# Performance work log

Measured on AMD Instinct MI355X. Metric: run time of the kernel, lower is better.

## Reference

```python
import jax, jax.numpy as jnp
import numpy as np

HEAD_COUNT = 16
HEAD_DIM = 128  # embed_count // head_count = 2048 // 16


def setup_inputs() -> dict:
    key = jax.random.key(0)
    k0, k1, k2, k3, k4 = jax.random.split(key, 5)
    B, C, S = 4, 2048, 1024
    keys = jax.random.normal(k0, (B, C, 1, S), dtype=jnp.float32)
    values = jax.random.normal(k1, (B, C, 1, S), dtype=jnp.float32)
    queries = jax.random.normal(k2, (B, C, 1, S), dtype=jnp.float32)
    attention_mask = jax.random.randint(k3, (B, S), 0, 2).astype(bool)
    # guarantee at least one valid key per batch row so softmax is finite
    attention_mask = attention_mask.at[:, 0].set(True)
    w_out = jax.random.normal(k4, (C, C), dtype=jnp.float32) * 0.02
    return {"keys": keys, "values": values, "queries": queries,
            "attention_mask": attention_mask, "w_out": w_out}


def reference(keys, values, queries, attention_mask, w_out):
    B, C, _, S = keys.shape
    h, d = HEAD_COUNT, HEAD_DIM
    # keys: [B,C,1,S] -> transpose(1,3) -> [B,S,1,C] -> [B,S,h,d]
    k = jnp.transpose(keys[:, :, 0, :], (0, 2, 1)).reshape(B, S, h, d)      # bkhd
    # values/queries: [B,C,1,S] -> [B,h,d,S] -> transpose(1,2) -> [B,d,h,S]
    v = jnp.transpose(values[:, :, 0, :].reshape(B, h, d, S), (0, 2, 1, 3))  # bdhk
    q = jnp.transpose(queries[:, :, 0, :].reshape(B, h, d, S), (0, 2, 1, 3)) # bdhq
    # additive mask bias: 0 where attended, -inf where masked; broadcast over h,q
    bias = jnp.where(attention_mask, 0.0, -jnp.inf).astype(keys.dtype)       # [B,K]
    scale = 1.0 / np.sqrt(d).astype(np.float32)
    w = jnp.einsum('bdhq,bkhd->bkhq', q * scale, k)                          # [B,K,h,Q]
    w = w + bias[:, :, None, None]
    w = jax.nn.softmax(w, axis=1)  # softmax over keys (dim 1)
    hid = jnp.einsum('bkhq,bdhk->bdhq', w, v)                                # [B,d,h,Q]
    hid = jnp.transpose(hid, (0, 2, 1, 3)).reshape(B, C, S)                  # [B,C,Q]
    out = jnp.einsum('oc,bcq->boq', w_out, hid)                              # 1x1 conv out_proj
    return out.reshape(B, C, 1, S)
```

## Files before the change

### kernel.cpp

```cpp
#include <hip/hip_runtime.h>

#define Bq 4
#define Cc 2048
#define Ss 1024
#define Hh 16
#define Dd 128

#define QSCALE 0.127517429f

typedef __bf16 bf16x8 __attribute__((ext_vector_type(8)));
typedef float  f32x4  __attribute__((ext_vector_type(4)));

__device__ __forceinline__ ushort f2bf(float f) {
    uint u = __float_as_uint(f);
    u += 0x7FFFu + ((u >> 16) & 1u);
    return (ushort)(u >> 16);
}
__device__ __forceinline__ uint pack2bf(float a, float b) {
    return (uint)f2bf(a) | ((uint)f2bf(b) << 16);
}
__device__ __forceinline__ void gld16(const void* g, void* l) {
    __builtin_amdgcn_global_load_lds(
        (const __attribute__((address_space(1))) unsigned int*)g,
        (__attribute__((address_space(3))) unsigned int*)l, 16, 0, 0);
}

__global__ __launch_bounds__(256) void mask_bias_k(const unsigned* __restrict__ mask,
                                                   float* __restrict__ bias) {
    __shared__ int f01, ff;
    const int t = threadIdx.x;
    if (t == 0) { f01 = 0; ff = 0; }
    __syncthreads();
    int a = 0, b = 0;
    for (int i = t; i < 1024; i += 256) {
        unsigned v = mask[i];
        if (v != 0u && v != 1u) a = 1;
        if (v != 0u && v != 0x3F800000u) b = 1;
    }
    if (a) atomicOr(&f01, 1);
    if (b) atomicOr(&ff, 1);
    __syncthreads();
    const int mode = f01 ? (ff ? 1 : 2) : 0;
    const int* mi = (const int*)mask;
    const unsigned char* mb = (const unsigned char*)mask;
    const float* mf = (const float*)mask;
    for (int i = t; i < Bq * Ss; i += 256) {
        bool on;
        if (mode == 0)      on = (mi[i] != 0);
        else if (mode == 1) on = (mb[i] != 0);
        else                on = (mf[i] != 0.0f);
        bias[i] = on ? 0.0f : -1e30f;
    }
}

__global__ __launch_bounds__(256) void wcvt_swz(const float* __restrict__ w,
                                                ushort* __restrict__ wb) {
    const size_t e = ((size_t)blockIdx.x * 256 + threadIdx.x) * 8;
    const int row = (int)(e >> 11), col = (int)(e & 2047);
    const int colS = (col & ~63) | ((col & 63) ^ ((row & 7) << 3));
    float4 v0 = *(const float4*)&w[e];
    float4 v1 = *(const float4*)&w[e + 4];
    uint4 o;
    o.x = pack2bf(v0.x, v0.y); o.y = pack2bf(v0.z, v0.w);
    o.z = pack2bf(v1.x, v1.y); o.w = pack2bf(v1.z, v1.w);
    *(uint4*)&wb[(size_t)row * 2048 + colS] = o;
}

__global__ __launch_bounds__(256) void vcvt_perm(const float* __restrict__ v,
                                                 ushort* __restrict__ vb) {
    const int tid = blockIdx.x * 256 + threadIdx.x;
    const int row = tid >> 7;
    const int cp = tid & 127;
    const int blk = (cp >> 3) * 64, x = cp & 7, kk0 = 2 * x;
    const float* src = v + (size_t)row * 1024 + blk;
    float a0 = src[kk0], a1 = src[16 + kk0], a2 = src[32 + kk0], a3 = src[48 + kk0];
    float b0 = src[kk0 + 1], b1 = src[17 + kk0], b2 = src[33 + kk0], b3 = src[49 + kk0];
    uint4 o;
    o.x = pack2bf(a0, a1); o.y = pack2bf(a2, a3);
    o.z = pack2bf(b0, b1); o.w = pack2bf(b2, b3);
    *(uint4*)&vb[(size_t)row * 1024 + blk + ((kk0 * 4) ^ ((row & 7) << 3))] = o;
}

__global__ __launch_bounds__(256) void qk_prep(const float* __restrict__ queries,
                                               const float* __restrict__ keys,
                                               ushort* __restrict__ Qt,
                                               ushort* __restrict__ Kt) {
    __shared__ float T[128][65];
    const int t = threadIdx.x;
    const int s0 = blockIdx.x * 64;
    const int bh = blockIdx.y;
    const int isK = blockIdx.z;
    const float* src = (isK ? keys : queries) + (size_t)bh * 128 * 1024;
    const float sc = isK ? 1.0f : QSCALE;

#pragma unroll
    for (int p = 0; p < 8; ++p) {
        const int d = p * 16 + (t >> 4);
        float4 v = *(const float4*)&src[(size_t)d * 1024 + s0 + (t & 15) * 4];
        T[d][(t & 15) * 4 + 0] = v.x * sc;
        T[d][(t & 15) * 4 + 1] = v.y * sc;
        T[d][(t & 15) * 4 + 2] = v.z * sc;
        T[d][(t & 15) * 4 + 3] = v.w * sc;
    }
    __syncthreads();

    ushort* outp = isK ? Kt : Qt;
#pragma unroll
    for (int p = 0; p < 4; ++p) {
        const int k = p * 16 + (t >> 4);
        const int x = t & 15;
        uint4 o;
        o.x = pack2bf(T[x * 8 + 0][k], T[x * 8 + 1][k]);
        o.y = pack2bf(T[x * 8 + 2][k], T[x * 8 + 3][k]);
        o.z = pack2bf(T[x * 8 + 4][k], T[x * 8 + 5][k]);
        o.w = pack2bf(T[x * 8 + 6][k], T[x * 8 + 7][k]);
        const size_t rowbyte = ((size_t)bh * 1024 + s0 + k) * 256;
        const int boff = isK ? ((x * 16) ^ ((k & 7) << 4)) : (x * 16);
        *(uint4*)((char*)outp + rowbyte + boff) = o;
    }
}

__global__ __launch_bounds__(512) void attn3(const ushort* __restrict__ Qt,
                                             const ushort* __restrict__ Kt,
                                             const ushort* __restrict__ Vbf,
                                             const float* __restrict__ bias,
                                             ushort* __restrict__ hidT) {
    __shared__ __align__(16) char SMEM[103424];
    ushort* KT2  = (ushort*)SMEM;
    ushort* Vs2  = (ushort*)(SMEM + 32768);
    ushort* PTb  = (ushort*)(SMEM + 65536);
    float*  biasS = (float*)(SMEM + 98304);
    float*  lbuf  = (float*)(SMEM + 102400);

    const int t = threadIdx.x, l = t & 63, w = t >> 6;
    const int kk = l & 15, g = l >> 4;

    const int bid = blockIdx.x;
    const int vid = (bid & 7) * 32 + (bid >> 3);
    const int bh = vid >> 2, qt = vid & 3;
    const int b = bh >> 4;
    const int q0 = qt * 256;
    const size_t bhbase = (size_t)bh * 1024;

    for (int i = t; i < Ss; i += 512) biasS[i] = bias[b * Ss + i];

    bf16x8 qf[2][4];
#pragma unroll
    for (int qs = 0; qs < 2; ++qs) {
        const ushort* qrow = Qt + (bhbase + q0 + w * 32 + qs * 16 + kk) * 128;
#pragma unroll
        for (int dc = 0; dc < 4; ++dc)
            qf[qs][dc] = *(const bf16x8*)(qrow + dc * 32 + g * 8);
    }

    ushort* pt = PTb + w * 2048;
    float lrun[2][4];
    f32x4 hacc[2][8];
#pragma unroll
    for (int qs = 0; qs < 2; ++qs) {
#pragma unroll
        for (int r = 0; r < 4; ++r) lrun[qs][r] = 0.0f;
#pragma unroll
        for (int i = 0; i < 8; ++i) hacc[qs][i] = (f32x4){0.f, 0.f, 0.f, 0.f};
    }

#define ATTN_STAGE(bufi, cki)                                                   \
    {                                                                           \
        const int k0n = (cki) * 64;                                             \
        _Pragma("unroll")                                                       \
        for (int ii = 0; ii < 2; ++ii) {                                        \
            const int ik = ii * 8 + w;                                          \
            gld16(Kt + (bhbase + k0n + ik * 4 + (l >> 4)) * 128 + (l & 15) * 8, \
                  KT2 + (bufi) * 8192 + ik * 512);                              \
            gld16(Vbf + ((size_t)bh * 128 + ik * 8 + (l >> 3)) * 1024 + k0n +   \
                      (l & 7) * 8,                                              \
                  Vs2 + (bufi) * 8192 + ik * 512);                              \
        }                                                                       \
    }

    ATTN_STAGE(0, 0);
    __syncthreads();

    int buf = 0;
    for (int ck = 0; ck < 16; ++ck) {
        const int k0 = ck * 64;
        if (ck + 1 < 16) ATTN_STAGE(buf ^ 1, ck + 1);

        const ushort* KTb = KT2 + buf * 8192;
        const ushort* Vsb = Vs2 + buf * 8192;

        float bk[4];
#pragma unroll
        for (int ns = 0; ns < 4; ++ns) bk[ns] = biasS[k0 + ns * 16 + kk];

        f32x4 sc[2][4];
#pragma unroll
        for (int ns = 0; ns < 4; ++ns) {
            bf16x8 kf[4];
            const ushort* kr = KTb + (ns * 16 + kk) * 128;
#pragma unroll
            for (int dc = 0; dc < 4; ++dc)
                kf[dc] = *(const bf16x8*)(kr + ((dc * 32 + g * 8) ^ ((kk & 7) << 3)));
#pragma unroll
            for (int qs = 0; qs < 2; ++qs) {
                f32x4 a = (f32x4){0.f, 0.f, 0.f, 0.f};
#pragma unroll
                for (int dc = 0; dc < 4; ++dc)
                    a = __builtin_amdgcn_mfma_f32_16x16x32_bf16(qf[qs][dc], kf[dc], a, 0, 0, 0);
                sc[qs][ns] = a;
            }
        }

#pragma unroll
        for (int qs = 0; qs < 2; ++qs)
#pragma unroll
            for (int r = 0; r < 4; ++r) {
                float p0 = exp2f(sc[qs][0][r] + bk[0]);
                float p1 = exp2f(sc[qs][1][r] + bk[1]);
                float p2 = exp2f(sc[qs][2][r] + bk[2]);
                float p3 = exp2f(sc[qs][3][r] + bk[3]);
                lrun[qs][r] += (p0 + p1) + (p2 + p3);
                const int row = qs * 16 + g * 4 + r;
                uint2 pk;
                pk.x = pack2bf(p0, p1); pk.y = pack2bf(p2, p3);
                *(uint2*)&pt[row * 64 + ((kk * 4) ^ ((row & 7) << 3))] = pk;
            }

#pragma unroll
        for (int kh = 0; kh < 2; ++kh) {
            bf16x8 pb[2];
#pragma unroll
            for (int qs = 0; qs < 2; ++qs)
                pb[qs] = *(const bf16x8*)(pt + (qs * 16 + kk) * 64 +
                                          ((kh * 32 + g * 8) ^ ((kk & 7) << 3)));
#pragma unroll
            for (int ds = 0; ds < 8; ++ds) {
                bf16x8 vf = *(const bf16x8*)(Vsb + (ds * 16 + kk) * 64 +
                                             ((kh * 32 + g * 8) ^ ((kk & 7) << 3)));
                hacc[0][ds] = __builtin_amdgcn_mfma_f32_16x16x32_bf16(vf, pb[0], hacc[0][ds], 0, 0, 0);
                hacc[1][ds] = __builtin_amdgcn_mfma_f32_16x16x32_bf16(vf, pb[1], hacc[1][ds], 0, 0, 0);
            }
        }

        asm volatile("s_waitcnt vmcnt(0)" ::: "memory");
        __builtin_amdgcn_s_barrier();
        buf ^= 1;
    }
#undef ATTN_STAGE

#pragma unroll
    for (int qs = 0; qs < 2; ++qs)
#pragma unroll
        for (int r = 0; r < 4; ++r) {
            float s = lrun[qs][r];
            s += __shfl_xor(s, 1); s += __shfl_xor(s, 2);
            s += __shfl_xor(s, 4); s += __shfl_xor(s, 8);
            if (kk == 0) lbuf[w * 32 + qs * 16 + g * 4 + r] = s;
        }
    float linv[2];
#pragma unroll
    for (int qs = 0; qs < 2; ++qs) linv[qs] = 1.0f / lbuf[w * 32 + qs * 16 + kk];

    __syncthreads();
    {
        ushort* hs = (ushort*)SMEM;
#pragma unroll
        for (int qs = 0; qs < 2; ++qs) {
            const int row = w * 32 + qs * 16 + kk;
#pragma unroll
            for (int ds = 0; ds < 8; ++ds) {
                uint2 pk;
                pk.x = pack2bf(hacc[qs][ds][0] * linv[qs], hacc[qs][ds][1] * linv[qs]);
                pk.y = pack2bf(hacc[qs][ds][2] * linv[qs], hacc[qs][ds][3] * linv[qs]);
                const int off = row * 256 + ((ds * 32 + g * 8) ^ ((row & 7) << 4));
                *(uint2*)((char*)hs + off) = pk;
            }
        }
    }
    __syncthreads();

    const int hh = bh & 15;
    const char* hsb = (const char*)SMEM;
#pragma unroll
    for (int it = 0; it < 8; ++it) {
        const int idx = it * 512 + t;
        const int q = idx >> 4, x = idx & 15;
        uint4 vv = *(const uint4*)(hsb + q * 256 + x * 16);
        *(uint4*)((char*)hidT + ((size_t)(b * Ss + q0 + q)) * 4096 + hh * 256 + x * 16) = vv;
    }
}

__global__ __launch_bounds__(512, 4) void proj2(const ushort* __restrict__ Wbf,
                                                const ushort* __restrict__ hidT,
                                                float* __restrict__ out) {
    __shared__ __align__(16) ushort Wl[2][128 * 64];
    __shared__ __align__(16) ushort Hl[2][128 * 64];
    const int t = threadIdx.x, l = t & 63, w = t >> 6;
    const int kk = l & 15, g = l >> 4;
    const int wr = w >> 2, wc = w & 3;

    const int bid = blockIdx.x;
    const int vid = (bid & 7) * 64 + (bid >> 3);
    const int o0 = (vid & 15) * 128;
    const int n0 = (vid >> 4) * 128;

    f32x4 acc[4][2];
#pragma unroll
    for (int i = 0; i < 4; ++i)
#pragma unroll
        for (int j = 0; j < 2; ++j) acc[i][j] = (f32x4){0.f, 0.f, 0.f, 0.f};

#define PROJ_STAGE(buf, ks)                                                        \
    {                                                                              \
        _Pragma("unroll")                                                          \
        for (int ii = 0; ii < 4; ++ii) {                                           \
            const int inst = ii * 8 + w;                                           \
            if (inst < 16) {                                                       \
                const int r = inst * 8 + (l >> 3);                                 \
                gld16(Wbf + ((size_t)(o0 + r) * Cc + (ks) * 64) + (l & 7) * 8,     \
                      &Wl[buf][inst * 512]);                                       \
            } else {                                                               \
                const int i2 = inst - 16;                                          \
                const int r = i2 * 8 + (l >> 3);                                   \
                gld16(hidT + ((size_t)(n0 + r) * Cc + (ks) * 64) + (l & 7) * 8,    \
                      &Hl[buf][i2 * 512]);                                         \
            }                                                                      \
        }                                                                          \
    }

    PROJ_STAGE(0, 0);
    asm volatile("s_waitcnt vmcnt(0)" ::: "memory");
    __builtin_amdgcn_s_barrier();

    int cur = 0;
    for (int ks = 0; ks < 32; ++ks) {
        if (ks + 1 < 32) PROJ_STAGE(cur ^ 1, ks + 1);
        bf16x8 af[2][4], bf[2][2];
#pragma unroll
        for (int dc = 0; dc < 2; ++dc) {
#pragma unroll
            for (int ms = 0; ms < 4; ++ms) {
                const int row = wr * 64 + ms * 16 + kk;
                af[dc][ms] = *(const bf16x8*)&Wl[cur][row * 64 +
                                 ((dc * 32 + g * 8) ^ ((kk & 7) << 3))];
            }
#pragma unroll
            for (int ns = 0; ns < 2; ++ns) {
                const int row = wc * 32 + ns * 16 + kk;
                bf[dc][ns] = *(const bf16x8*)&Hl[cur][row * 64 +
                                 ((dc * 32 + g * 8) ^ ((kk & 7) << 3))];
            }
        }
#pragma unroll
        for (int dc = 0; dc < 2; ++dc)
#pragma unroll
            for (int ms = 0; ms < 4; ++ms)
#pragma unroll
                for (int ns = 0; ns < 2; ++ns)
                    acc[ms][ns] = __builtin_amdgcn_mfma_f32_16x16x32_bf16(
                        af[dc][ms], bf[dc][ns], acc[ms][ns], 0, 0, 0);
        asm volatile("s_waitcnt vmcnt(0) lgkmcnt(0)" ::: "memory");
        __builtin_amdgcn_s_barrier();
        cur ^= 1;
    }
#undef PROJ_STAGE

#pragma unroll
    for (int ms = 0; ms < 4; ++ms)
#pragma unroll
        for (int ns = 0; ns < 2; ++ns) {
            const int o = o0 + wr * 64 + ms * 16 + g * 4;
            const int n = n0 + wc * 32 + ns * 16 + kk;
            const int bb = n >> 10, qq = n & 1023;
            float* op = out + ((size_t)(bb * Cc + o)) * Ss + qq;
#pragma unroll
            for (int r = 0; r < 4; ++r) op[(size_t)r * Ss] = acc[ms][ns][r];
        }
}

extern "C" void kernel_launch(void* const* d_in, const int* in_sizes, int n_in,
                              void* d_out, int out_size, void* d_ws, size_t ws_size,
                              hipStream_t stream) {
    const float*    keys    = (const float*)d_in[0];
    const float*    values  = (const float*)d_in[1];
    const float*    queries = (const float*)d_in[2];
    const unsigned* mask    = (const unsigned*)d_in[3];
    const float*    w_out   = (const float*)d_in[4];
    float* out = (float*)d_out;

    char* ws = (char*)d_ws;
    float*  bias = (float*)ws;
    ushort* Wbf  = (ushort*)(ws + 16384);
    ushort* Qt   = (ushort*)(ws + 16384 + (8u << 20));
    ushort* Kt   = (ushort*)(ws + 16384 + (24u << 20));
    ushort* Vbf  = (ushort*)(ws + 16384 + (40u << 20));
    ushort* hidT = (ushort*)(ws + 16384 + (56u << 20));

    hipLaunchKernelGGL(mask_bias_k, dim3(1), dim3(256), 0, stream, mask, bias);
    hipLaunchKernelGGL(wcvt_swz, dim3(2048), dim3(256), 0, stream, w_out, Wbf);
    hipLaunchKernelGGL(vcvt_perm, dim3(4096), dim3(256), 0, stream, values, Vbf);
    hipLaunchKernelGGL(qk_prep, dim3(16, 64, 2), dim3(256), 0, stream,
                       queries, keys, Qt, Kt);
    hipLaunchKernelGGL(attn3, dim3(256), dim3(512), 0, stream,
                       Qt, Kt, Vbf, bias, hidT);
    hipLaunchKernelGGL(proj2, dim3(512), dim3(512), 0, stream,
                       Wbf, hidT, out);
}
```

Measured before the change: 131.8 us.

## Keep softmax probabilities in registers via transposed QK MFMA, shrink attention blocks

The QK^T MFMA operands are swapped so the score tile comes out transposed, which lets the exponentiated probabilities be packed straight into bf16 B-operand fragments for the PV MFMA. This removes the LDS round trip for P and the cross-lane row-sum reduction through LDS. The attention kernel now uses 256-thread blocks covering 128 queries over 512 blocks, with less shared memory, to raise occupancy. The V conversion kernel is rewritten to use vectorized float4 loads matching the new key permutation, and s_setprio hints are placed around the MFMA sections. The layout change has to line up exactly with the MFMA fragment mapping, and the smaller blocks load each K/V tile twice as often.

Measured after the change: 129.4 us. About the same (-1.8%).

```diff
diff --git a/kernel.cpp b/kernel.cpp
--- a/kernel.cpp
+++ b/kernel.cpp
@@ -71,14 +71,16 @@
     const int tid = blockIdx.x * 256 + threadIdx.x;
     const int row = tid >> 7;
     const int cp = tid & 127;
-    const int blk = (cp >> 3) * 64, x = cp & 7, kk0 = 2 * x;
-    const float* src = v + (size_t)row * 1024 + blk;
-    float a0 = src[kk0], a1 = src[16 + kk0], a2 = src[32 + kk0], a3 = src[48 + kk0];
-    float b0 = src[kk0 + 1], b1 = src[17 + kk0], b2 = src[33 + kk0], b3 = src[49 + kk0];
+    const int blk = (cp >> 3) * 64;
+    const int j0 = cp & 7;
+    const int b5 = j0 >> 2, h = j0 & 3;
+    const float* src = v + (size_t)row * 1024 + blk + 32 * b5 + 4 * h;
+    float4 A = *(const float4*)src;
+    float4 B = *(const float4*)(src + 16);
     uint4 o;
-    o.x = pack2bf(a0, a1); o.y = pack2bf(a2, a3);
-    o.z = pack2bf(b0, b1); o.w = pack2bf(b2, b3);
-    *(uint4*)&vb[(size_t)row * 1024 + blk + ((kk0 * 4) ^ ((row & 7) << 3))] = o;
+    o.x = pack2bf(A.x, A.y); o.y = pack2bf(A.z, A.w);
+    o.z = pack2bf(B.x, B.y); o.w = pack2bf(B.z, B.w);
+    *(uint4*)&vb[(size_t)row * 1024 + blk + ((j0 * 8) ^ ((row & 7) << 3))] = o;
 }
 
 __global__ __launch_bounds__(256) void qk_prep(const float* __restrict__ queries,
@@ -120,29 +122,27 @@
     }
 }
 
-__global__ __launch_bounds__(512) void attn3(const ushort* __restrict__ Qt,
+__global__ __launch_bounds__(256) void attn4(const ushort* __restrict__ Qt,
                                              const ushort* __restrict__ Kt,
                                              const ushort* __restrict__ Vbf,
                                              const float* __restrict__ bias,
                                              ushort* __restrict__ hidT) {
-    __shared__ __align__(16) char SMEM[103424];
+    __shared__ __align__(16) char SMEM[69632];
     ushort* KT2  = (ushort*)SMEM;
     ushort* Vs2  = (ushort*)(SMEM + 32768);
-    ushort* PTb  = (ushort*)(SMEM + 65536);
-    float*  biasS = (float*)(SMEM + 98304);
-    float*  lbuf  = (float*)(SMEM + 102400);
+    float*  biasS = (float*)(SMEM + 65536);
 
     const int t = threadIdx.x, l = t & 63, w = t >> 6;
     const int kk = l & 15, g = l >> 4;
 
     const int bid = blockIdx.x;
-    const int vid = (bid & 7) * 32 + (bid >> 3);
-    const int bh = vid >> 2, qt = vid & 3;
+    const int vid = (bid & 7) * 64 + (bid >> 3);
+    const int bh = vid >> 3, qt = vid & 7;
     const int b = bh >> 4;
-    const int q0 = qt * 256;
+    const int q0 = qt * 128;
     const size_t bhbase = (size_t)bh * 1024;
 
-    for (int i = t; i < Ss; i += 512) biasS[i] = bias[b * Ss + i];
+    for (int i = t; i < Ss; i += 256) biasS[i] = bias[b * Ss + i];
 
     bf16x8 qf[2][4];
 #pragma unroll
@@ -153,23 +153,19 @@
             qf[qs][dc] = *(const bf16x8*)(qrow + dc * 32 + g * 8);
     }
 
-    ushort* pt = PTb + w * 2048;
-    float lrun[2][4];
+    float lrun[2] = {0.0f, 0.0f};
     f32x4 hacc[2][8];
 #pragma unroll
-    for (int qs = 0; qs < 2; ++qs) {
-#pragma unroll
-        for (int r = 0; r < 4; ++r) lrun[qs][r] = 0.0f;
+    for (int qs = 0; qs < 2; ++qs)
 #pragma unroll
         for (int i = 0; i < 8; ++i) hacc[qs][i] = (f32x4){0.f, 0.f, 0.f, 0.f};
-    }
 
 #define ATTN_STAGE(bufi, cki)                                                   \
     {                                                                           \
         const int k0n = (cki) * 64;                                             \
         _Pragma("unroll")                                                       \
-        for (int ii = 0; ii < 2; ++ii) {                                        \
-            const int ik = ii * 8 + w;                                          \
+        for (int ii = 0; ii < 4; ++ii) {                                        \
+            const int ik = ii * 4 + w;                                          \
             gld16(Kt + (bhbase + k0n + ik * 4 + (l >> 4)) * 128 + (l & 15) * 8, \
                   KT2 + (bufi) * 8192 + ik * 512);                              \
             gld16(Vbf + ((size_t)bh * 128 + ik * 8 + (l >> 3)) * 1024 + k0n +   \
@@ -189,11 +185,8 @@
         const ushort* KTb = KT2 + buf * 8192;
         const ushort* Vsb = Vs2 + buf * 8192;
 
-        float bk[4];
-#pragma unroll
-        for (int ns = 0; ns < 4; ++ns) bk[ns] = biasS[k0 + ns * 16 + kk];
-
         f32x4 sc[2][4];
+        __builtin_amdgcn_s_setprio(1);
 #pragma unroll
         for (int ns = 0; ns < 4; ++ns) {
             bf16x8 kf[4];
@@ -206,41 +199,55 @@
                 f32x4 a = (f32x4){0.f, 0.f, 0.f, 0.f};
 #pragma unroll
                 for (int dc = 0; dc < 4; ++dc)
-                    a = __builtin_amdgcn_mfma_f32_16x16x32_bf16(qf[qs][dc], kf[dc], a, 0, 0, 0);
+                    a = __builtin_amdgcn_mfma_f32_16x16x32_bf16(kf[dc], qf[qs][dc], a, 0, 0, 0);
                 sc[qs][ns] = a;
             }
         }
-
-#pragma unroll
-        for (int qs = 0; qs < 2; ++qs)
-#pragma unroll
-            for (int r = 0; r < 4; ++r) {
-                float p0 = exp2f(sc[qs][0][r] + bk[0]);
-                float p1 = exp2f(sc[qs][1][r] + bk[1]);
-                float p2 = exp2f(sc[qs][2][r] + bk[2]);
-                float p3 = exp2f(sc[qs][3][r] + bk[3]);
-                lrun[qs][r] += (p0 + p1) + (p2 + p3);
-                const int row = qs * 16 + g * 4 + r;
-                uint2 pk;
-                pk.x = pack2bf(p0, p1); pk.y = pack2bf(p2, p3);
-                *(uint2*)&pt[row * 64 + ((kk * 4) ^ ((row & 7) << 3))] = pk;
-            }
-
+        __builtin_amdgcn_s_setprio(0);
+
+        float4 bk4[4];
+#pragma unroll
+        for (int ns = 0; ns < 4; ++ns)
+            bk4[ns] = *(const float4*)&biasS[k0 + ns * 16 + g * 4];
+
+        bf16x8 pb[2][2];
+#pragma unroll
+        for (int qs = 0; qs < 2; ++qs) {
+            float pv[4][4];
+            float s = 0.0f;
+#pragma unroll
+            for (int ns = 0; ns < 4; ++ns) {
+                const float* bb = (const float*)&bk4[ns];
+#pragma unroll
+                for (int r = 0; r < 4; ++r) {
+                    float p = exp2f(sc[qs][ns][r] + bb[r]);
+                    pv[ns][r] = p;
+                    s += p;
+                }
+            }
+            lrun[qs] += s;
+#pragma unroll
+            for (int kh = 0; kh < 2; ++kh) {
+                bf16x8 vpk;
+#pragma unroll
+                for (int j = 0; j < 8; ++j)
+                    vpk[j] = (__bf16)pv[2 * kh + (j >> 2)][j & 3];
+                pb[qs][kh] = vpk;
+            }
+        }
+
+        __builtin_amdgcn_s_setprio(1);
 #pragma unroll
         for (int kh = 0; kh < 2; ++kh) {
-            bf16x8 pb[2];
-#pragma unroll
-            for (int qs = 0; qs < 2; ++qs)
-                pb[qs] = *(const bf16x8*)(pt + (qs * 16 + kk) * 64 +
-                                          ((kh * 32 + g * 8) ^ ((kk & 7) << 3)));
 #pragma unroll
             for (int ds = 0; ds < 8; ++ds) {
                 bf16x8 vf = *(const bf16x8*)(Vsb + (ds * 16 + kk) * 64 +
                                              ((kh * 32 + g * 8) ^ ((kk & 7) << 3)));
-                hacc[0][ds] = __builtin_amdgcn_mfma_f32_16x16x32_bf16(vf, pb[0], hacc[0][ds], 0, 0, 0);
-                hacc[1][ds] = __builtin_amdgcn_mfma_f32_16x16x32_bf16(vf, pb[1], hacc[1][ds], 0, 0, 0);
-            }
-        }
+                hacc[0][ds] = __builtin_amdgcn_mfma_f32_16x16x32_bf16(vf, pb[0][kh], hacc[0][ds], 0, 0, 0);
+                hacc[1][ds] = __builtin_amdgcn_mfma_f32_16x16x32_bf16(vf, pb[1][kh], hacc[1][ds], 0, 0, 0);
+            }
+        }
+        __builtin_amdgcn_s_setprio(0);
 
         asm volatile("s_waitcnt vmcnt(0)" ::: "memory");
         __builtin_amdgcn_s_barrier();
@@ -248,20 +255,15 @@
     }
 #undef ATTN_STAGE
 
-#pragma unroll
-    for (int qs = 0; qs < 2; ++qs)
-#pragma unroll
-        for (int r = 0; r < 4; ++r) {
-            float s = lrun[qs][r];
-            s += __shfl_xor(s, 1); s += __shfl_xor(s, 2);
-            s += __shfl_xor(s, 4); s += __shfl_xor(s, 8);
-            if (kk == 0) lbuf[w * 32 + qs * 16 + g * 4 + r] = s;
-        }
     float linv[2];
 #pragma unroll
-    for (int qs = 0; qs < 2; ++qs) linv[qs] = 1.0f / lbuf[w * 32 + qs * 16 + kk];
-
-    __syncthreads();
+    for (int qs = 0; qs < 2; ++qs) {
+        float s = lrun[qs];
+        s += __shfl_xor(s, 16);
+        s += __shfl_xor(s, 32);
+        linv[qs] = 1.0f / s;
+    }
+
     {
         ushort* hs = (ushort*)SMEM;
 #pragma unroll
@@ -283,7 +285,7 @@
     const char* hsb = (const char*)SMEM;
 #pragma unroll
     for (int it = 0; it < 8; ++it) {
-        const int idx = it * 512 + t;
+        const int idx = it * 256 + t;
         const int q = idx >> 4, x = idx & 15;
         uint4 vv = *(const uint4*)(hsb + q * 256 + x * 16);
         *(uint4*)((char*)hidT + ((size_t)(b * Ss + q0 + q)) * 4096 + hh * 256 + x * 16) = vv;
@@ -351,6 +353,7 @@
                                  ((dc * 32 + g * 8) ^ ((kk & 7) << 3))];
             }
         }
+        __builtin_amdgcn_s_setprio(1);
 #pragma unroll
         for (int dc = 0; dc < 2; ++dc)
 #pragma unroll
@@ -359,6 +362,7 @@
                 for (int ns = 0; ns < 2; ++ns)
                     acc[ms][ns] = __builtin_amdgcn_mfma_f32_16x16x32_bf16(
                         af[dc][ms], bf[dc][ns], acc[ms][ns], 0, 0, 0);
+        __builtin_amdgcn_s_setprio(0);
         asm volatile("s_waitcnt vmcnt(0) lgkmcnt(0)" ::: "memory");
         __builtin_amdgcn_s_barrier();
         cur ^= 1;
@@ -401,7 +405,7 @@
     hipLaunchKernelGGL(vcvt_perm, dim3(4096), dim3(256), 0, stream, values, Vbf);
     hipLaunchKernelGGL(qk_prep, dim3(16, 64, 2), dim3(256), 0, stream,
                        queries, keys, Qt, Kt);
-    hipLaunchKernelGGL(attn3, dim3(256), dim3(512), 0, stream,
+    hipLaunchKernelGGL(attn4, dim3(512), dim3(256), 0, stream,
                        Qt, Kt, Vbf, bias, hidT);
     hipLaunchKernelGGL(proj2, dim3(512), dim3(512), 0, stream,
                        Wbf, hidT, out);
```
